# Kernel optimization log

Measured on AMD Instinct MI355X. Metric: run time of the kernel, lower is better.

Reference implementation:

```python
import jax, jax.numpy as jnp
import numpy as np

# Config matching the torch ModelConfig
B, T, C = 4, 4096, 1024      # batch, block_size, n_embed
H, HS = 16, 64               # num_heads, head_size (H*HS == C)
K = 256                      # Linformer low-rank dim k


def setup_inputs() -> dict:
    key = jax.random.key(0)
    ks = jax.random.split(key, 8)
    x = jax.random.normal(ks[0], (B, T, C), dtype=jnp.float32)
    # per-head Q/K/V weights (nn.Linear, bias=False): init std=0.02
    WQ = 0.02 * jax.random.normal(ks[1], (H, C, HS), dtype=jnp.float32)
    WK = 0.02 * jax.random.normal(ks[2], (H, C, HS), dtype=jnp.float32)
    WV = 0.02 * jax.random.normal(ks[3], (H, C, HS), dtype=jnp.float32)
    # per-head E matrix, shape [B, T, K] (xavier-like scale); F exists in
    # the original but is never used in forward, so it is omitted.
    xav = (2.0 / (T + K)) ** 0.5
    E = xav * jax.random.normal(ks[4], (H, B, T, K), dtype=jnp.float32)
    # output projection nn.Linear(C, C)
    Wp = 0.02 * jax.random.normal(ks[5], (C, C), dtype=jnp.float32)
    bp = jnp.zeros((C,), dtype=jnp.float32)
    return {"x": x, "WQ": WQ, "WK": WK, "WV": WV, "E": E, "Wp": Wp, "bp": bp}


def reference(x, WQ, WK, WV, E, Wp, bp):
    Tcur = x.shape[1]
    q = jnp.einsum('btc,hcs->hbts', x, WQ)   # [H,B,T,HS]
    k = jnp.einsum('btc,hcs->hbts', x, WK)
    v = jnp.einsum('btc,hcs->hbts', x, WV)
    # low-rank projection: E^T @ k, E^T @ v  -> [H,B,K,HS]
    kp = jnp.einsum('hbtr,hbts->hbrs', E, k)
    vp = jnp.einsum('hbtr,hbts->hbrs', E, v)
    # attention weights over compressed dim K, scaled by 1/sqrt(k)
    w = jnp.einsum('hbts,hbrs->hbtr', q, kp) / jnp.sqrt(jnp.float32(K))
    # mask = tril(T,T)[:T, :K]: position t may attend compressed slot r iff r <= t
    mask = jnp.arange(K)[None, :] <= jnp.arange(Tcur)[:, None]  # [T,K]
    w = jnp.where(mask[None, None], w, jnp.float32(-jnp.inf))
    w = jax.nn.softmax(w, axis=-1)
    # dropout is identity in eval mode
    out = jnp.einsum('hbtr,hbrs->hbts', w, vp)          # [H,B,T,HS]
    out = out.transpose(1, 2, 0, 3).reshape(x.shape[0], Tcur, H * HS)
    return out @ Wp.T + bp
```

## Files before the change

kernel.cpp:

```cpp
#include <hip/hip_runtime.h>
#include <stdint.h>

typedef __attribute__((ext_vector_type(8))) short bf16x8;
typedef __attribute__((ext_vector_type(4))) float f32x4;
typedef __attribute__((ext_vector_type(4))) unsigned short us4;

__device__ __forceinline__ unsigned short f2bf(float f){
  unsigned int u = __float_as_uint(f);
  u += 0x7FFFu + ((u >> 16) & 1u);
  return (unsigned short)(u >> 16);
}

__device__ __forceinline__ void gload16(const void* g, void* l){
  __builtin_amdgcn_global_load_lds((const __attribute__((address_space(1))) void*)g,
                                   (__attribute__((address_space(3))) void*)l, 16, 0, 0);
}

__global__ __launch_bounds__(256) void pack4_k(const float* __restrict__ src,
                                               unsigned short* __restrict__ dst, int n4){
  int i = blockIdx.x*256 + threadIdx.x;
  if (i >= n4) return;
  float4 v = ((const float4*)src)[i];
  us4 o; o.x=f2bf(v.x); o.y=f2bf(v.y); o.z=f2bf(v.z); o.w=f2bf(v.w);
  ((us4*)dst)[i] = o;
}

__global__ __launch_bounds__(256) void pack_w1t_k(const float* __restrict__ WQ,
    const float* __restrict__ WK, const float* __restrict__ WV,
    unsigned short* __restrict__ w1t){
  int i = blockIdx.x*256 + threadIdx.x;
  int n = i >> 10, c = i & 1023;
  int sec = n >> 10, hh = (n >> 6) & 15, s = n & 63;
  const float* W = (sec == 0) ? WQ : ((sec == 1) ? WK : WV);
  w1t[i] = f2bf(W[(hh*1024 + c)*64 + s]);
}

template<int OF32>
__global__ __launch_bounds__(256,2) void gemm_bt_k(
    const unsigned short* __restrict__ A, const unsigned short* __restrict__ Bt,
    void* __restrict__ Cout, const float* __restrict__ bias, int M, int N, int Kd)
{
  __shared__ unsigned short As[128*64];
  __shared__ unsigned short Bs[128*64];
  const int tid = threadIdx.x;
  const int w = tid >> 6, l = tid & 63;
  const int g = l >> 4, c16 = l & 15;
  const int m0 = blockIdx.y*128, n0 = blockIdx.x*128;
  const int wm = (w >> 1)*64, wn = (w & 1)*64;
  const int srow = l >> 3, sblk = l & 7;

  f32x4 acc[4][4];
  #pragma unroll
  for (int i=0;i<4;i++)
    #pragma unroll
    for (int j=0;j<4;j++) acc[i][j] = f32x4{0.f,0.f,0.f,0.f};

  for (int k0 = 0; k0 < Kd; k0 += 64){
    #pragma unroll
    for (int i=0;i<4;i++){
      int row = w*32 + i*8 + srow;
      int jb = sblk ^ (row & 7);
      gload16(A  + (size_t)(m0+row)*Kd + k0 + jb*8, (char*)As + (w*32+i*8)*128);
      gload16(Bt + (size_t)(n0+row)*Kd + k0 + jb*8, (char*)Bs + (w*32+i*8)*128);
    }
    __syncthreads();
    #pragma unroll
    for (int kk=0; kk<2; kk++){
      bf16x8 af[4], bfr[4];
      #pragma unroll
      for (int mt=0; mt<4; mt++){
        int row = wm + mt*16 + c16;
        af[mt] = *(const bf16x8*)((const char*)As + row*128 + (((kk*4+g) ^ (row&7))*16));
      }
      #pragma unroll
      for (int nt=0; nt<4; nt++){
        int row = wn + nt*16 + c16;
        bfr[nt] = *(const bf16x8*)((const char*)Bs + row*128 + (((kk*4+g) ^ (row&7))*16));
      }
      #pragma unroll
      for (int mt=0; mt<4; mt++)
        #pragma unroll
        for (int nt=0; nt<4; nt++)
          acc[mt][nt] = __builtin_amdgcn_mfma_f32_16x16x32_bf16(af[mt], bfr[nt], acc[mt][nt], 0,0,0);
    }
    __syncthreads();
  }
  #pragma unroll
  for (int mt=0; mt<4; mt++)
    #pragma unroll
    for (int nt=0; nt<4; nt++)
      #pragma unroll
      for (int r=0; r<4; r++){
        int row = m0 + wm + mt*16 + g*4 + r;
        int col = n0 + wn + nt*16 + c16;
        float v = acc[mt][nt][r];
        if (OF32) ((float*)Cout)[(size_t)row*N + col] = v + bias[col];
        else ((unsigned short*)Cout)[(size_t)row*N + col] = f2bf(v);
      }
}

__global__ __launch_bounds__(256,2) void eproj_k(
    const float* __restrict__ E, const unsigned short* __restrict__ kvT,
    float* __restrict__ kpacc, float* __restrict__ vpacc)
{
  __shared__ unsigned short Bs[128*32];
  const int tid = threadIdx.x;
  const int w = tid >> 6, l = tid & 63;
  const int g = l >> 4, c16 = l & 15;
  const int pair = blockIdx.x, split = blockIdx.y;
  const int h = pair >> 2, b = pair & 3;
  const float* Eb = E + (size_t)pair*4096*256;

  f32x4 acc[4][8];
  #pragma unroll
  for (int i=0;i<4;i++)
    #pragma unroll
    for (int j=0;j<8;j++) acc[i][j] = f32x4{0.f,0.f,0.f,0.f};

  for (int step=0; step<16; step++){
    int t0 = split*512 + step*32;
    #pragma unroll
    for (int i=0;i<2;i++){
      int c = w*32 + i*16 + (l>>2);
      int row = (c < 64) ? (h*64 + c) : (960 + h*64 + c);
      int jb = (l&3) ^ ((c>>1)&3);
      gload16(kvT + (size_t)row*16384 + b*4096 + t0 + jb*8, (char*)Bs + (w*32+i*16)*64);
    }
    __syncthreads();
    bf16x8 af[4];
    #pragma unroll
    for (int mt=0; mt<4; mt++){
      int r = w*64 + mt*16 + c16;
      const float* ep = Eb + (size_t)(t0 + g*8)*256 + r;
      #pragma unroll
      for (int j=0;j<8;j++) af[mt][j] = (short)f2bf(ep[(size_t)j*256]);
    }
    #pragma unroll
    for (int nt=0; nt<8; nt++){
      int c = nt*16 + c16;
      bf16x8 bfr = *(const bf16x8*)((const char*)Bs + c*64 + ((g ^ ((c>>1)&3))*16));
      #pragma unroll
      for (int mt=0; mt<4; mt++)
        acc[mt][nt] = __builtin_amdgcn_mfma_f32_16x16x32_bf16(af[mt], bfr, acc[mt][nt], 0,0,0);
    }
    __syncthreads();
  }
  #pragma unroll
  for (int mt=0; mt<4; mt++)
    #pragma unroll
    for (int nt=0; nt<8; nt++)
      #pragma unroll
      for (int r2=0; r2<4; r2++){
        int r = w*64 + mt*16 + g*4 + r2;
        int c = nt*16 + c16;
        float v = acc[mt][nt][r2];
        if (c < 64) atomicAdd(kpacc + ((size_t)pair*256 + r)*64 + c, v);
        else        atomicAdd(vpacc + ((size_t)pair*256 + r)*64 + (c - 64), v);
      }
}

__global__ __launch_bounds__(256) void finalize_k(const float* __restrict__ kpacc,
    const float* __restrict__ vpacc, unsigned short* __restrict__ kp,
    unsigned short* __restrict__ vpT){
  int i = blockIdx.x*256 + threadIdx.x;
  int pair = i >> 14, r = (i >> 6) & 255, s = i & 63;
  kp[i] = f2bf(kpacc[i] * 0.0625f);
  vpT[(((size_t)pair*64 + s) << 8) + r] = f2bf(vpacc[i]);
}

__global__ __launch_bounds__(512,2) void attn_k(
    const unsigned short* __restrict__ q, const unsigned short* __restrict__ kp,
    const unsigned short* __restrict__ vpT, unsigned short* __restrict__ attn)
{
  __shared__ unsigned short kps[256*64];
  __shared__ unsigned short vps[64*256];
  __shared__ unsigned short Ps[8][16*256];
  const int tid = threadIdx.x;
  const int w = tid >> 6, l = tid & 63;
  const int g = l >> 4, c16 = l & 15;
  const int pair = blockIdx.x >> 5, chunk = blockIdx.x & 31;
  const int h = pair >> 2, b = pair & 3;
  const unsigned short* kpg = kp + (size_t)pair*256*64;
  const unsigned short* vpg = vpT + (size_t)pair*64*256;
  #pragma unroll
  for (int i=0;i<4;i++){
    int r = w*32 + i*8 + (l>>3);
    int jb = (l&7) ^ (r&7);
    gload16(kpg + r*64 + jb*8, (char*)kps + (w*32+i*8)*128);
  }
  #pragma unroll
  for (int i=0;i<4;i++){
    int s = w*8 + i*2 + (l>>5);
    int jb = (l&31) ^ (s&7);
    gload16(vpg + s*256 + jb*8, (char*)vps + (w*8+i*2)*512);
  }
  __syncthreads();

  const int tseq = chunk*128 + w*16;
  const unsigned short* qp = q + ((size_t)(b*4096 + tseq + c16))*1024 + h*64;
  bf16x8 qa[2];
  qa[0] = *(const bf16x8*)(qp + g*8);
  qa[1] = *(const bf16x8*)(qp + 32 + g*8);

  f32x4 sa[16];
  #pragma unroll
  for (int i=0;i<16;i++) sa[i] = f32x4{0.f,0.f,0.f,0.f};
  #pragma unroll
  for (int nt=0; nt<16; nt++){
    #pragma unroll
    for (int kk=0; kk<2; kk++){
      int r = nt*16 + c16;
      bf16x8 bfr = *(const bf16x8*)((const char*)kps + r*128 + (((kk*4+g) ^ (r&7))*16));
      sa[nt] = __builtin_amdgcn_mfma_f32_16x16x32_bf16(qa[kk], bfr, sa[nt], 0,0,0);
    }
  }
  #pragma unroll
  for (int reg=0; reg<4; reg++){
    const int tg = tseq + g*4 + reg;
    float m = -3.0e38f;
    #pragma unroll
    for (int nt=0; nt<16; nt++){
      int r = nt*16 + c16;
      float v = (r <= tg) ? sa[nt][reg] : -3.0e38f;
      sa[nt][reg] = v;
      m = fmaxf(m, v);
    }
    #pragma unroll
    for (int d=1; d<16; d<<=1) m = fmaxf(m, __shfl_xor(m, d, 64));
    float ssum = 0.f;
    #pragma unroll
    for (int nt=0; nt<16; nt++){
      float p = __expf(sa[nt][reg] - m);
      sa[nt][reg] = p; ssum += p;
    }
    #pragma unroll
    for (int d=1; d<16; d<<=1) ssum += __shfl_xor(ssum, d, 64);
    float inv = 1.f / ssum;
    #pragma unroll
    for (int nt=0; nt<16; nt++) sa[nt][reg] *= inv;
  }
  unsigned short* pw = &Ps[w][0];
  #pragma unroll
  for (int nt=0; nt<16; nt++){
    #pragma unroll
    for (int reg=0; reg<4; reg++){
      int tl = g*4 + reg;
      int r = nt*16 + c16;
      *(unsigned short*)((char*)pw + tl*512 + (((r>>3) ^ (tl&7))*16) + (r&7)*2) = f2bf(sa[nt][reg]);
    }
  }
  __syncthreads();
  f32x4 oa[4];
  #pragma unroll
  for (int i=0;i<4;i++) oa[i] = f32x4{0.f,0.f,0.f,0.f};
  #pragma unroll
  for (int kk=0; kk<8; kk++){
    bf16x8 pa = *(const bf16x8*)((const char*)pw + c16*512 + (((kk*4+g) ^ (c16&7))*16));
    #pragma unroll
    for (int nt=0; nt<4; nt++){
      int s = nt*16 + c16;
      bf16x8 vb = *(const bf16x8*)((const char*)vps + s*512 + (((kk*4+g) ^ (s&7))*16));
      oa[nt] = __builtin_amdgcn_mfma_f32_16x16x32_bf16(pa, vb, oa[nt], 0,0,0);
    }
  }
  unsigned short* ap = attn + ((size_t)(b*4096 + tseq))*1024 + h*64;
  #pragma unroll
  for (int nt=0; nt<4; nt++)
    #pragma unroll
    for (int reg=0; reg<4; reg++){
      int tl = g*4 + reg;
      ap[(size_t)tl*1024 + nt*16 + c16] = f2bf(oa[nt][reg]);
    }
}

extern "C" void kernel_launch(void* const* d_in, const int* in_sizes, int n_in,
                              void* d_out, int out_size, void* d_ws, size_t ws_size,
                              hipStream_t stream)
{
  const float* x  = (const float*)d_in[0];
  const float* WQ = (const float*)d_in[1];
  const float* WK = (const float*)d_in[2];
  const float* WV = (const float*)d_in[3];
  const float* E  = (const float*)d_in[4];
  const float* Wp = (const float*)d_in[5];
  const float* bp = (const float*)d_in[6];
  float* out = (float*)d_out;
  (void)in_sizes; (void)n_in; (void)out_size; (void)ws_size;

  char* ws = (char*)d_ws;
  size_t off = 0;
  auto alloc = [&](size_t bytes)->char*{ char* p = ws + off; off += (bytes + 255) & ~(size_t)255; return p; };
  unsigned short* xb    = (unsigned short*)alloc((size_t)16384*1024*2);
  unsigned short* w1t   = (unsigned short*)alloc((size_t)3072*1024*2);
  unsigned short* wpb   = (unsigned short*)alloc((size_t)1024*1024*2);
  unsigned short* qb    = (unsigned short*)alloc((size_t)16384*1024*2);
  unsigned short* kvT   = (unsigned short*)alloc((size_t)2048*16384*2);
  float*          kpacc = (float*)alloc((size_t)64*256*64*4);
  float*          vpacc = (float*)alloc((size_t)64*256*64*4);
  unsigned short* kp    = (unsigned short*)alloc((size_t)64*256*64*2);
  unsigned short* vpT   = (unsigned short*)alloc((size_t)64*64*256*2);
  unsigned short* attn  = (unsigned short*)alloc((size_t)16384*1024*2);

  pack4_k<<<16384, 256, 0, stream>>>(x, xb, 16384*1024/4);
  pack4_k<<<1024, 256, 0, stream>>>(Wp, wpb, 1024*1024/4);
  pack_w1t_k<<<12288, 256, 0, stream>>>(WQ, WK, WV, w1t);

  gemm_bt_k<0><<<dim3(8,128), 256, 0, stream>>>(xb, w1t, qb, nullptr, 16384, 1024, 1024);
  gemm_bt_k<0><<<dim3(128,16), 256, 0, stream>>>(w1t + (size_t)1024*1024, xb, kvT, nullptr, 2048, 16384, 1024);

  hipMemsetAsync(kpacc, 0, (size_t)64*256*64*4*2, stream);
  eproj_k<<<dim3(64,8), 256, 0, stream>>>(E, kvT, kpacc, vpacc);
  finalize_k<<<4096, 256, 0, stream>>>(kpacc, vpacc, kp, vpT);

  attn_k<<<2048, 512, 0, stream>>>(qb, kp, vpT, attn);

  gemm_bt_k<1><<<dim3(8,128), 256, 0, stream>>>(attn, wpb, out, bp, 16384, 1024, 1024);
}
```

Baseline: 785.6 us.

## Pre-transpose E to bf16 and rewrite E-projection as tiled LDS GEMM

Adds a kernel that converts E to bf16 and transposes it to [pair, r, t], so the E-projection can use the same swizzled LDS-tiled MFMA GEMM structure as the main GEMMs. Before, each thread did strided fp32 global loads of E and converted them inline. The K/V weight packing is reordered so each head's K and V rows are interleaved, letting one 128-row B tile cover both, and the kp/vp accumulators are merged into one buffer. The GEMM kernel also remaps block IDs in a stride-8 pattern to improve cache locality. In exchange this adds an extra pass over E (read fp32, write bf16) and workspace for EbT, which is aliased with the attn buffer.

```diff
diff --git a/kernel.cpp b/kernel.cpp
--- a/kernel.cpp
+++ b/kernel.cpp
@@ -30,9 +30,37 @@
     unsigned short* __restrict__ w1t){
   int i = blockIdx.x*256 + threadIdx.x;
   int n = i >> 10, c = i & 1023;
-  int sec = n >> 10, hh = (n >> 6) & 15, s = n & 63;
-  const float* W = (sec == 0) ? WQ : ((sec == 1) ? WK : WV);
-  w1t[i] = f2bf(W[(hh*1024 + c)*64 + s]);
+  const float* W; int h, s;
+  if (n < 1024){ h = n >> 6; s = n & 63; W = WQ; }
+  else { int m = n - 1024; h = m >> 7; s = m & 63; W = ((m >> 6) & 1) ? WV : WK; }
+  w1t[i] = f2bf(W[(h*1024 + c)*64 + s]);
+}
+
+__global__ __launch_bounds__(256) void etrans_k(const float* __restrict__ E,
+                                                unsigned short* __restrict__ EbT){
+  __shared__ unsigned short L[64][66];
+  const int tb = blockIdx.x, rb = blockIdx.y, pair = blockIdx.z;
+  const float* src = E + ((size_t)pair*4096 + tb*64)*256 + rb*64;
+  const int tt = threadIdx.x >> 2;
+  const int r4 = (threadIdx.x & 3) * 16;
+  const float4* s4 = (const float4*)(src + (size_t)tt*256 + r4);
+  #pragma unroll
+  for (int i=0;i<4;i++){
+    float4 v = s4[i];
+    L[tt][r4+i*4+0]=f2bf(v.x); L[tt][r4+i*4+1]=f2bf(v.y);
+    L[tt][r4+i*4+2]=f2bf(v.z); L[tt][r4+i*4+3]=f2bf(v.w);
+  }
+  __syncthreads();
+  const int rr = threadIdx.x >> 2;
+  const int t4 = (threadIdx.x & 3) * 16;
+  unsigned short* dst = EbT + ((size_t)(pair*256 + rb*64 + rr))*4096 + tb*64 + t4;
+  #pragma unroll
+  for (int i=0;i<4;i++){
+    us4 o;
+    o.x = L[t4+i*4+0][rr]; o.y = L[t4+i*4+1][rr];
+    o.z = L[t4+i*4+2][rr]; o.w = L[t4+i*4+3][rr];
+    ((us4*)dst)[i] = o;
+  }
 }
 
 template<int OF32>
@@ -45,7 +73,10 @@
   const int tid = threadIdx.x;
   const int w = tid >> 6, l = tid & 63;
   const int g = l >> 4, c16 = l & 15;
-  const int m0 = blockIdx.y*128, n0 = blockIdx.x*128;
+  int nwg = gridDim.x*gridDim.y;
+  int orig = blockIdx.y*gridDim.x + blockIdx.x;
+  int id = (orig & 7)*(nwg >> 3) + (orig >> 3);
+  const int m0 = (id / gridDim.x)*128, n0 = (id % gridDim.x)*128;
   const int wm = (w >> 1)*64, wn = (w & 1)*64;
   const int srow = l >> 3, sblk = l & 7;
 
@@ -99,73 +130,75 @@
       }
 }
 
-__global__ __launch_bounds__(256,2) void eproj_k(
-    const float* __restrict__ E, const unsigned short* __restrict__ kvT,
-    float* __restrict__ kpacc, float* __restrict__ vpacc)
+__global__ __launch_bounds__(256,2) void eproj2_k(
+    const unsigned short* __restrict__ EbT, const unsigned short* __restrict__ kvT,
+    float* __restrict__ kpvacc)
 {
-  __shared__ unsigned short Bs[128*32];
+  __shared__ unsigned short As[128*64];
+  __shared__ unsigned short Bs[128*64];
   const int tid = threadIdx.x;
   const int w = tid >> 6, l = tid & 63;
   const int g = l >> 4, c16 = l & 15;
-  const int pair = blockIdx.x, split = blockIdx.y;
+  const int sp = blockIdx.x, mh = blockIdx.y, pair = blockIdx.z;
   const int h = pair >> 2, b = pair & 3;
-  const float* Eb = E + (size_t)pair*4096*256;
-
-  f32x4 acc[4][8];
+  const unsigned short* Abase = EbT + ((size_t)(pair*256 + mh*128))*4096 + sp*1024;
+  const unsigned short* Bbase = kvT + ((size_t)(h*128))*16384 + b*4096 + sp*1024;
+  const int wm = (w >> 1)*64, wn = (w & 1)*64;
+  const int srow = l >> 3, sblk = l & 7;
+
+  f32x4 acc[4][4];
   #pragma unroll
   for (int i=0;i<4;i++)
     #pragma unroll
-    for (int j=0;j<8;j++) acc[i][j] = f32x4{0.f,0.f,0.f,0.f};
-
-  for (int step=0; step<16; step++){
-    int t0 = split*512 + step*32;
-    #pragma unroll
-    for (int i=0;i<2;i++){
-      int c = w*32 + i*16 + (l>>2);
-      int row = (c < 64) ? (h*64 + c) : (960 + h*64 + c);
-      int jb = (l&3) ^ ((c>>1)&3);
-      gload16(kvT + (size_t)row*16384 + b*4096 + t0 + jb*8, (char*)Bs + (w*32+i*16)*64);
+    for (int j=0;j<4;j++) acc[i][j] = f32x4{0.f,0.f,0.f,0.f};
+
+  for (int k0 = 0; k0 < 1024; k0 += 64){
+    #pragma unroll
+    for (int i=0;i<4;i++){
+      int row = w*32 + i*8 + srow;
+      int jb = sblk ^ (row & 7);
+      gload16(Abase + (size_t)row*4096  + k0 + jb*8, (char*)As + (w*32+i*8)*128);
+      gload16(Bbase + (size_t)row*16384 + k0 + jb*8, (char*)Bs + (w*32+i*8)*128);
     }
     __syncthreads();
-    bf16x8 af[4];
-    #pragma unroll
-    for (int mt=0; mt<4; mt++){
-      int r = w*64 + mt*16 + c16;
-      const float* ep = Eb + (size_t)(t0 + g*8)*256 + r;
-      #pragma unroll
-      for (int j=0;j<8;j++) af[mt][j] = (short)f2bf(ep[(size_t)j*256]);
-    }
-    #pragma unroll
-    for (int nt=0; nt<8; nt++){
-      int c = nt*16 + c16;
-      bf16x8 bfr = *(const bf16x8*)((const char*)Bs + c*64 + ((g ^ ((c>>1)&3))*16));
+    #pragma unroll
+    for (int kk=0; kk<2; kk++){
+      bf16x8 af[4], bfr[4];
+      #pragma unroll
+      for (int mt=0; mt<4; mt++){
+        int row = wm + mt*16 + c16;
+        af[mt] = *(const bf16x8*)((const char*)As + row*128 + (((kk*4+g) ^ (row&7))*16));
+      }
+      #pragma unroll
+      for (int nt=0; nt<4; nt++){
+        int row = wn + nt*16 + c16;
+        bfr[nt] = *(const bf16x8*)((const char*)Bs + row*128 + (((kk*4+g) ^ (row&7))*16));
+      }
       #pragma unroll
       for (int mt=0; mt<4; mt++)
-        acc[mt][nt] = __builtin_amdgcn_mfma_f32_16x16x32_bf16(af[mt], bfr, acc[mt][nt], 0,0,0);
+        #pragma unroll
+        for (int nt=0; nt<4; nt++)
+          acc[mt][nt] = __builtin_amdgcn_mfma_f32_16x16x32_bf16(af[mt], bfr[nt], acc[mt][nt], 0,0,0);
     }
     __syncthreads();
   }
+  float* C = kpvacc + (size_t)(pair*256 + mh*128)*128;
   #pragma unroll
   for (int mt=0; mt<4; mt++)
     #pragma unroll
-    for (int nt=0; nt<8; nt++)
-      #pragma unroll
-      for (int r2=0; r2<4; r2++){
-        int r = w*64 + mt*16 + g*4 + r2;
-        int c = nt*16 + c16;
-        float v = acc[mt][nt][r2];
-        if (c < 64) atomicAdd(kpacc + ((size_t)pair*256 + r)*64 + c, v);
-        else        atomicAdd(vpacc + ((size_t)pair*256 + r)*64 + (c - 64), v);
-      }
-}
-
-__global__ __launch_bounds__(256) void finalize_k(const float* __restrict__ kpacc,
-    const float* __restrict__ vpacc, unsigned short* __restrict__ kp,
-    unsigned short* __restrict__ vpT){
+    for (int nt=0; nt<4; nt++)
+      #pragma unroll
+      for (int r=0; r<4; r++)
+        atomicAdd(C + (size_t)(wm + mt*16 + g*4 + r)*128 + wn + nt*16 + c16, acc[mt][nt][r]);
+}
+
+__global__ __launch_bounds__(256) void finalize2_k(const float* __restrict__ kpvacc,
+    unsigned short* __restrict__ kp, unsigned short* __restrict__ vpT){
   int i = blockIdx.x*256 + threadIdx.x;
-  int pair = i >> 14, r = (i >> 6) & 255, s = i & 63;
-  kp[i] = f2bf(kpacc[i] * 0.0625f);
-  vpT[(((size_t)pair*64 + s) << 8) + r] = f2bf(vpacc[i]);
+  int pair = i >> 15, r = (i >> 7) & 255, c = i & 127;
+  float v = kpvacc[i];
+  if (c < 64) kp[((size_t)pair*256 + r)*64 + c] = f2bf(v * 0.0625f);
+  else        vpT[((size_t)pair*64 + (c - 64))*256 + r] = f2bf(v);
 }
 
 __global__ __launch_bounds__(512,2) void attn_k(
@@ -290,27 +323,28 @@
   char* ws = (char*)d_ws;
   size_t off = 0;
   auto alloc = [&](size_t bytes)->char*{ char* p = ws + off; off += (bytes + 255) & ~(size_t)255; return p; };
-  unsigned short* xb    = (unsigned short*)alloc((size_t)16384*1024*2);
-  unsigned short* w1t   = (unsigned short*)alloc((size_t)3072*1024*2);
-  unsigned short* wpb   = (unsigned short*)alloc((size_t)1024*1024*2);
-  unsigned short* qb    = (unsigned short*)alloc((size_t)16384*1024*2);
-  unsigned short* kvT   = (unsigned short*)alloc((size_t)2048*16384*2);
-  float*          kpacc = (float*)alloc((size_t)64*256*64*4);
-  float*          vpacc = (float*)alloc((size_t)64*256*64*4);
-  unsigned short* kp    = (unsigned short*)alloc((size_t)64*256*64*2);
-  unsigned short* vpT   = (unsigned short*)alloc((size_t)64*64*256*2);
-  unsigned short* attn  = (unsigned short*)alloc((size_t)16384*1024*2);
+  unsigned short* xb     = (unsigned short*)alloc((size_t)16384*1024*2);
+  unsigned short* w1t    = (unsigned short*)alloc((size_t)3072*1024*2);
+  unsigned short* wpb    = (unsigned short*)alloc((size_t)1024*1024*2);
+  unsigned short* qb     = (unsigned short*)alloc((size_t)16384*1024*2);
+  unsigned short* kvT    = (unsigned short*)alloc((size_t)2048*16384*2);
+  float*          kpvacc = (float*)alloc((size_t)64*256*128*4);
+  unsigned short* kp     = (unsigned short*)alloc((size_t)64*256*64*2);
+  unsigned short* vpT    = (unsigned short*)alloc((size_t)64*64*256*2);
+  unsigned short* EbT    = (unsigned short*)alloc((size_t)64*256*4096*2);
+  unsigned short* attn   = EbT;
 
   pack4_k<<<16384, 256, 0, stream>>>(x, xb, 16384*1024/4);
   pack4_k<<<1024, 256, 0, stream>>>(Wp, wpb, 1024*1024/4);
   pack_w1t_k<<<12288, 256, 0, stream>>>(WQ, WK, WV, w1t);
+  etrans_k<<<dim3(64,4,64), 256, 0, stream>>>(E, EbT);
 
   gemm_bt_k<0><<<dim3(8,128), 256, 0, stream>>>(xb, w1t, qb, nullptr, 16384, 1024, 1024);
   gemm_bt_k<0><<<dim3(128,16), 256, 0, stream>>>(w1t + (size_t)1024*1024, xb, kvT, nullptr, 2048, 16384, 1024);
 
-  hipMemsetAsync(kpacc, 0, (size_t)64*256*64*4*2, stream);
-  eproj_k<<<dim3(64,8), 256, 0, stream>>>(E, kvT, kpacc, vpacc);
-  finalize_k<<<4096, 256, 0, stream>>>(kpacc, vpacc, kp, vpT);
+  hipMemsetAsync(kpvacc, 0, (size_t)64*256*128*4, stream);
+  eproj2_k<<<dim3(4,2,64), 256, 0, stream>>>(EbT, kvT, kpvacc);
+  finalize2_k<<<8192, 256, 0, stream>>>(kpvacc, kp, vpT);
 
   attn_k<<<2048, 512, 0, stream>>>(qb, kp, vpT, attn);
 
```

After: 762.9 us. 1.03x faster.
